# Kernel tuning notes

Hardware: AMD Instinct MI355X
Metric: run time of the kernel (lower is better)

Reference implementation:

```python
import jax, jax.numpy as jnp
import numpy as np

BLOCK = 64  # block_size from config
NEG_INF = -1e9


def setup_inputs() -> dict:
    key = jax.random.key(0)
    k1, k2, k3, k4 = jax.random.split(key, 4)
    B, H, S, D = 2, 8, 2048, 64
    nb = S // BLOCK  # 32 blocks per side
    query = jax.random.normal(k1, (B, H, S, D), dtype=jnp.float32)
    key_t = jax.random.normal(k2, (B, H, S, D), dtype=jnp.float32)
    value = jax.random.normal(k3, (B, H, S, D), dtype=jnp.float32)
    # binary block mask; force diagonal blocks on so every row has >=1 valid key
    mat = jax.random.randint(k4, (nb, nb), 0, 2).astype(jnp.int32)
    mat = mat.at[jnp.arange(nb), jnp.arange(nb)].set(1)
    mask = jnp.ones((B, S), dtype=jnp.float32)  # padding mask (1 = keep)
    return {"query": query, "key": key_t, "value": value, "mask": mask, "mat": mat}


def reference(query, key, value, mask, mat):
    # Upsample block mask [nb, nb] -> dense [S, S] (nearest, like nn.Upsample)
    block_dense = jnp.repeat(jnp.repeat(mat, BLOCK, axis=0), BLOCK, axis=1) > 0
    # Block-sparse QK^T: only positions inside nonzero blocks participate.
    scores = jnp.einsum('bhqd,bhkd->bhqk', query, key)
    # Additive padding-mask bias, as in the original: 1e6 * (1 - mask)
    scores = scores - 1e6 * (1.0 - mask)[:, None, None, :]
    # Positions outside the block pattern are excluded from the softmax.
    scores = jnp.where(block_dense[None, None, :, :], scores, NEG_INF)
    attn = jax.nn.softmax(scores, axis=-1)
    out = jnp.einsum('bhqk,bhkd->bhqd', attn, value)
    return out
```

## Files before the change

kernel.cpp:

```cpp
#include <hip/hip_runtime.h>


typedef __attribute__((ext_vector_type(8))) short short8;
typedef __attribute__((ext_vector_type(4))) short short4_;
typedef __attribute__((ext_vector_type(4))) float float4_;
typedef __attribute__((ext_vector_type(8))) _Float16 half8_;

#define B_   2
#define H_   8
#define S_   2048
#define D_   64
#define NB_  32
#define KP   72

__device__ __forceinline__ short f2bf(float f) {
    union { float f; unsigned int u; } x; x.f = f;
    unsigned int r = x.u + 0x7FFFu + ((x.u >> 16) & 1u);
    return (short)(r >> 16);
}
__device__ __forceinline__ float bf2f(short s) {
    union { unsigned int u; float f; } x; x.u = ((unsigned int)(unsigned short)s) << 16;
    return x.f;
}
__device__ __forceinline__ short f2h(float f) {
    _Float16 h = (_Float16)f;
    return __builtin_bit_cast(short, h);
}

__global__ __launch_bounds__(256)
void preconvert_kernel(const float* __restrict__ K, const float* __restrict__ V,
                       short* __restrict__ Khf, short* __restrict__ Vtb) {
    __shared__ short vn[64 * KP];
    const int tid = threadIdx.x;
    const int kt  = blockIdx.x;
    const int bh  = blockIdx.y;
    const size_t tb = ((size_t)bh * S_ + kt * 64) * D_;

#pragma unroll
    for (int it = 0; it < 4; ++it) {
        int i = tid + it * 256;
        int row = i >> 4, c4 = (i & 15) * 4;
        float4_ kv = *(const float4_*)(K + tb + row * D_ + c4);
        short4_ kh;
#pragma unroll
        for (int e = 0; e < 4; ++e) kh[e] = f2h(kv[e]);
        *(short4_*)(Khf + tb + row * D_ + c4) = kh;
        float4_ vv = *(const float4_*)(V + tb + row * D_ + c4);
        short4_ vb;
#pragma unroll
        for (int e = 0; e < 4; ++e) vb[e] = f2bf(vv[e]);
        *(short4_*)&vn[row * KP + c4] = vb;
    }
    __syncthreads();
#pragma unroll
    for (int it = 0; it < 2; ++it) {
        int i = tid + it * 256;
        int rowd = i >> 3, key8 = (i & 7) * 8;
        short8 o;
#pragma unroll
        for (int e = 0; e < 8; ++e) o[e] = vn[(key8 + e) * KP + rowd];
        *(short8*)(Vtb + (((size_t)(bh * NB_ + kt)) * 64 + rowd) * 64 + key8) = o;
    }
}

__global__ __launch_bounds__(128, 2)
void attn_mfma_h(const float* __restrict__ Q,
                 const float* __restrict__ Msk,
                 const int* __restrict__ Mat,
                 float* __restrict__ O,
                 const short* __restrict__ Khf_g,
                 const short* __restrict__ Vtb_g) {
    __shared__ __align__(16) short lds[(64 + 64 + 2 * 16) * KP];
    short* Kh = lds;
    short* Vt = lds + 64 * KP;
    short* Pl = lds + 2 * 64 * KP;

    const int tid  = threadIdx.x;
    const int wave = tid >> 6;
    const int lane = tid & 63;
    const int c    = lane & 15;
    const int quad = lane >> 4;

    const int qt = blockIdx.x;
    const int bh = blockIdx.y;
    const int b  = bh / H_;
    const int qb = qt >> 1;
    const size_t base = (size_t)bh * S_ * D_;

    half8_ qa0, qa1;
    {
        const float* qp = Q + base + (size_t)(qt * 32 + wave * 16 + c) * D_ + quad * 8;
#pragma unroll
        for (int e = 0; e < 8; ++e) {
            qa0[e] = (_Float16)qp[e];
            qa1[e] = (_Float16)qp[e + 32];
        }
    }

    float4_ o[4];
    float l_part[4];
#pragma unroll
    for (int t = 0; t < 4; ++t) { o[t][0] = 0.f; o[t][1] = 0.f; o[t][2] = 0.f; o[t][3] = 0.f; }
#pragma unroll
    for (int j = 0; j < 4; ++j) l_part[j] = 0.f;

    unsigned long long bm = __ballot(Mat[qb * NB_ + (lane & 31)] != 0);
    unsigned int mbits = (unsigned int)(bm & 0xFFFFFFFFull);

    int srow[4], scol[4];
#pragma unroll
    for (int it = 0; it < 4; ++it) {
        int i = tid + it * 128;
        srow[it] = i >> 3;
        scol[it] = (i & 7) * 8;
    }

    short8 sK[4], sV[4];
    float  biasn[4];

    int kb = __builtin_ctz(mbits);
    mbits &= mbits - 1;
    {
        const short* kh = Khf_g + base + (size_t)kb * 64 * D_;
        const short* vt = Vtb_g + ((size_t)(bh * NB_ + kb)) * 64 * 64;
#pragma unroll
        for (int it = 0; it < 4; ++it) {
            sK[it] = *(const short8*)(kh + srow[it] * 64 + scol[it]);
            sV[it] = *(const short8*)(vt + srow[it] * 64 + scol[it]);
        }
#pragma unroll
        for (int t = 0; t < 4; ++t)
            biasn[t] = -1.0e6f * (1.0f - Msk[(size_t)b * S_ + kb * 64 + t * 16 + c]);
    }

    for (;;) {
        __syncthreads();
#pragma unroll
        for (int it = 0; it < 4; ++it) {
            *(short8*)&Kh[srow[it] * KP + scol[it]] = sK[it];
            *(short8*)&Vt[srow[it] * KP + scol[it]] = sV[it];
        }
        float biasc[4];
#pragma unroll
        for (int t = 0; t < 4; ++t) biasc[t] = biasn[t];
        __syncthreads();

        const bool have_next = (mbits != 0);
        if (have_next) {
            kb = __builtin_ctz(mbits);
            mbits &= mbits - 1;
            const short* kh = Khf_g + base + (size_t)kb * 64 * D_;
            const short* vt = Vtb_g + ((size_t)(bh * NB_ + kb)) * 64 * 64;
#pragma unroll
            for (int it = 0; it < 4; ++it) {
                sK[it] = *(const short8*)(kh + srow[it] * 64 + scol[it]);
                sV[it] = *(const short8*)(vt + srow[it] * 64 + scol[it]);
            }
#pragma unroll
            for (int t = 0; t < 4; ++t)
                biasn[t] = -1.0e6f * (1.0f - Msk[(size_t)b * S_ + kb * 64 + t * 16 + c]);
        }

        float4_ sc[4];
#pragma unroll
        for (int t = 0; t < 4; ++t) { sc[t][0] = 0.f; sc[t][1] = 0.f; sc[t][2] = 0.f; sc[t][3] = 0.f; }
#pragma unroll
        for (int t = 0; t < 4; ++t) {
            const short* kp_ = &Kh[(t * 16 + c) * KP + quad * 8];
            half8_ kb0 = __builtin_bit_cast(half8_, *(const short8*)(kp_));
            half8_ kb1 = __builtin_bit_cast(half8_, *(const short8*)(kp_ + 32));
            sc[t] = __builtin_amdgcn_mfma_f32_16x16x32_f16(qa0, kb0, sc[t], 0, 0, 0);
            sc[t] = __builtin_amdgcn_mfma_f32_16x16x32_f16(qa1, kb1, sc[t], 0, 0, 0);
        }

        short* Pw = Pl + wave * 16 * KP;
#pragma unroll
        for (int t = 0; t < 4; ++t) {
#pragma unroll
            for (int j = 0; j < 4; ++j) {
                float p = __expf(sc[t][j] + biasc[t]);
                l_part[j] += p;
                Pw[(quad * 4 + j) * KP + t * 16 + c] = f2bf(p);
            }
        }

        const short* pp = Pl + wave * 16 * KP + c * KP + quad * 8;
        short8 pa0 = *(const short8*)(pp);
        short8 pa1 = *(const short8*)(pp + 32);

#pragma unroll
        for (int t = 0; t < 4; ++t) {
            const short* vp = &Vt[(t * 16 + c) * KP + quad * 8];
            short8 vb0 = *(const short8*)(vp);
            short8 vb1 = *(const short8*)(vp + 32);
            o[t] = __builtin_amdgcn_mfma_f32_16x16x32_bf16(pa0, vb0, o[t], 0, 0, 0);
            o[t] = __builtin_amdgcn_mfma_f32_16x16x32_bf16(pa1, vb1, o[t], 0, 0, 0);
        }

        if (!have_next) break;
    }

#pragma unroll
    for (int j = 0; j < 4; ++j) {
        float rs = l_part[j];
        rs += __shfl_xor(rs, 1);
        rs += __shfl_xor(rs, 2);
        rs += __shfl_xor(rs, 4);
        rs += __shfl_xor(rs, 8);
        float inv = 1.0f / rs;
        size_t rowoff = base + (size_t)(qt * 32 + wave * 16 + quad * 4 + j) * D_;
#pragma unroll
        for (int t = 0; t < 4; ++t)
            O[rowoff + t * 16 + c] = o[t][j] * inv;
    }
}

__global__ __launch_bounds__(256, 2)
void attn_mfma_fb(const float* __restrict__ Q,
                  const float* __restrict__ K,
                  const float* __restrict__ V,
                  const float* __restrict__ Msk,
                  const int* __restrict__ Mat,
                  float* __restrict__ O) {
    __shared__ __align__(16) short lds[4 * 64 * KP];
    short* Khi = lds;
    short* Klo = lds + 64 * KP;
    short* Vt  = lds + 2 * 64 * KP;
    short* Pl  = lds + 3 * 64 * KP;

    const int tid  = threadIdx.x;
    const int wave = tid >> 6;
    const int lane = tid & 63;
    const int c    = lane & 15;
    const int quad = lane >> 4;

    const int qb = blockIdx.x;
    const int bh = blockIdx.y;
    const int b  = bh / H_;
    const size_t base = (size_t)bh * S_ * D_;

    short8 qh0, qh1, ql0, ql1;
    {
        const float* qp = Q + base + (size_t)(qb * 64 + wave * 16 + c) * D_ + quad * 8;
#pragma unroll
        for (int e = 0; e < 8; ++e) {
            float f0 = qp[e], f1 = qp[e + 32];
            qh0[e] = f2bf(f0); ql0[e] = f2bf(f0 - bf2f(qh0[e]));
            qh1[e] = f2bf(f1); ql1[e] = f2bf(f1 - bf2f(qh1[e]));
        }
    }

    float4_ o[4];
    float l_part[4];
#pragma unroll
    for (int t = 0; t < 4; ++t) { o[t][0] = 0.f; o[t][1] = 0.f; o[t][2] = 0.f; o[t][3] = 0.f; }
#pragma unroll
    for (int j = 0; j < 4; ++j) l_part[j] = 0.f;

    for (int kb = 0; kb < NB_; ++kb) {
        if (Mat[qb * NB_ + kb] == 0) continue;

        __syncthreads();
        {
            const float* kg = K + base + (size_t)kb * 64 * D_;
            const float* vg = V + base + (size_t)kb * 64 * D_;
#pragma unroll
            for (int it = 0; it < 4; ++it) {
                int i = tid + it * 256;
                int row = i >> 4, c4 = (i & 15) * 4;
                float4_ kv = *(const float4_*)(kg + row * D_ + c4);
                short4_ hi, lo;
#pragma unroll
                for (int e = 0; e < 4; ++e) {
                    hi[e] = f2bf(kv[e]);
                    lo[e] = f2bf(kv[e] - bf2f(hi[e]));
                }
                *(short4_*)&Khi[row * KP + c4] = hi;
                *(short4_*)&Klo[row * KP + c4] = lo;
                float4_ vv = *(const float4_*)(vg + row * D_ + c4);
#pragma unroll
                for (int e = 0; e < 4; ++e) Vt[(c4 + e) * KP + row] = f2bf(vv[e]);
            }
        }
        __syncthreads();

        float4_ sc[4];
#pragma unroll
        for (int t = 0; t < 4; ++t) { sc[t][0] = 0.f; sc[t][1] = 0.f; sc[t][2] = 0.f; sc[t][3] = 0.f; }
#pragma unroll
        for (int t = 0; t < 4; ++t) {
            const short* kph = &Khi[(t * 16 + c) * KP + quad * 8];
            const short* kpl = &Klo[(t * 16 + c) * KP + quad * 8];
            short8 kh0 = *(const short8*)(kph);
            short8 kh1 = *(const short8*)(kph + 32);
            short8 kl0 = *(const short8*)(kpl);
            short8 kl1 = *(const short8*)(kpl + 32);
            sc[t] = __builtin_amdgcn_mfma_f32_16x16x32_bf16(qh0, kh0, sc[t], 0, 0, 0);
            sc[t] = __builtin_amdgcn_mfma_f32_16x16x32_bf16(qh1, kh1, sc[t], 0, 0, 0);
            sc[t] = __builtin_amdgcn_mfma_f32_16x16x32_bf16(qh0, kl0, sc[t], 0, 0, 0);
            sc[t] = __builtin_amdgcn_mfma_f32_16x16x32_bf16(qh1, kl1, sc[t], 0, 0, 0);
            sc[t] = __builtin_amdgcn_mfma_f32_16x16x32_bf16(ql0, kh0, sc[t], 0, 0, 0);
            sc[t] = __builtin_amdgcn_mfma_f32_16x16x32_bf16(ql1, kh1, sc[t], 0, 0, 0);
        }

        short* Pw = Pl + wave * 16 * KP;
#pragma unroll
        for (int t = 0; t < 4; ++t) {
            float bias = -1.0e6f * (1.0f - Msk[(size_t)b * S_ + kb * 64 + t * 16 + c]);
#pragma unroll
            for (int j = 0; j < 4; ++j) {
                float p = __expf(sc[t][j] + bias);
                l_part[j] += p;
                Pw[(quad * 4 + j) * KP + t * 16 + c] = f2bf(p);
            }
        }

        const short* pp = Pl + wave * 16 * KP + c * KP + quad * 8;
        short8 pa0 = *(const short8*)(pp);
        short8 pa1 = *(const short8*)(pp + 32);

#pragma unroll
        for (int t = 0; t < 4; ++t) {
            const short* vp = &Vt[(t * 16 + c) * KP + quad * 8];
            short8 vb0 = *(const short8*)(vp);
            short8 vb1 = *(const short8*)(vp + 32);
            o[t] = __builtin_amdgcn_mfma_f32_16x16x32_bf16(pa0, vb0, o[t], 0, 0, 0);
            o[t] = __builtin_amdgcn_mfma_f32_16x16x32_bf16(pa1, vb1, o[t], 0, 0, 0);
        }
    }

#pragma unroll
    for (int j = 0; j < 4; ++j) {
        float rs = l_part[j];
        rs += __shfl_xor(rs, 1);
        rs += __shfl_xor(rs, 2);
        rs += __shfl_xor(rs, 4);
        rs += __shfl_xor(rs, 8);
        float inv = 1.0f / rs;
        size_t rowoff = base + (size_t)(qb * 64 + wave * 16 + quad * 4 + j) * D_;
#pragma unroll
        for (int t = 0; t < 4; ++t)
            O[rowoff + t * 16 + c] = o[t][j] * inv;
    }
}

extern "C" void kernel_launch(void* const* d_in, const int* in_sizes, int n_in,
                              void* d_out, int out_size, void* d_ws, size_t ws_size,
                              hipStream_t stream) {
    const float* q   = (const float*)d_in[0];
    const float* k   = (const float*)d_in[1];
    const float* v   = (const float*)d_in[2];
    const float* msk = (const float*)d_in[3];
    const int*   mat = (const int*)d_in[4];
    float*       out = (float*)d_out;

    const size_t elems = (size_t)B_ * H_ * S_ * D_;
    const size_t need  = 2 * elems * sizeof(short);
    const int use_pre  = (ws_size >= need) ? 1 : 0;

    short* khf = (short*)d_ws;
    short* vtb = khf + elems;

    if (use_pre) {
        dim3 pgrid(NB_, B_ * H_);
        preconvert_kernel<<<pgrid, dim3(256), 0, stream>>>(k, v, khf, vtb);
        dim3 grid(S_ / 32, B_ * H_);
        attn_mfma_h<<<grid, dim3(128), 0, stream>>>(q, msk, mat, out, khf, vtb);
    } else {
        dim3 grid(NB_, B_ * H_);
        attn_mfma_fb<<<grid, dim3(256), 0, stream>>>(q, k, v, msk, mat, out);
    }
}
```

Baseline: 112.9 us.

## Double-buffer K/V tiles in LDS with XOR swizzle and exp2 softmax

Replaces the padded single-buffer LDS staging with two XOR-swizzled K/V buffers. The next tile is written into the alternate buffer after the current compute, so each iteration needs one barrier instead of two. The log2(e) factor is folded into the fp16 K conversion and the mask bias, which lets the kernel call exp2f in place of __expf. P is now converted to bf16 by truncation rather than round-to-nearest. LDS use grows, which may lower occupancy, and truncation slightly reduces accuracy.

```diff
diff --git a/kernel.cpp b/kernel.cpp
--- a/kernel.cpp
+++ b/kernel.cpp
@@ -12,12 +12,17 @@
 #define D_   64
 #define NB_  32
 #define KP   72
+#define LOG2E 1.4426950408889634f
 
 __device__ __forceinline__ short f2bf(float f) {
     union { float f; unsigned int u; } x; x.f = f;
     unsigned int r = x.u + 0x7FFFu + ((x.u >> 16) & 1u);
     return (short)(r >> 16);
 }
+__device__ __forceinline__ short f2bf_t(float f) {
+    union { float f; unsigned int u; } x; x.f = f;
+    return (short)(x.u >> 16);
+}
 __device__ __forceinline__ float bf2f(short s) {
     union { unsigned int u; float f; } x; x.u = ((unsigned int)(unsigned short)s) << 16;
     return x.f;
@@ -25,6 +30,9 @@
 __device__ __forceinline__ short f2h(float f) {
     _Float16 h = (_Float16)f;
     return __builtin_bit_cast(short, h);
+}
+__device__ __forceinline__ int swz(int row, int gran) {
+    return (row << 6) + (((gran ^ row) & 7) << 3);
 }
 
 __global__ __launch_bounds__(256)
@@ -43,7 +51,7 @@
         float4_ kv = *(const float4_*)(K + tb + row * D_ + c4);
         short4_ kh;
 #pragma unroll
-        for (int e = 0; e < 4; ++e) kh[e] = f2h(kv[e]);
+        for (int e = 0; e < 4; ++e) kh[e] = f2h(kv[e] * LOG2E);
         *(short4_*)(Khf + tb + row * D_ + c4) = kh;
         float4_ vv = *(const float4_*)(V + tb + row * D_ + c4);
         short4_ vb;
@@ -64,16 +72,13 @@
 }
 
 __global__ __launch_bounds__(128, 2)
-void attn_mfma_h(const float* __restrict__ Q,
-                 const float* __restrict__ Msk,
-                 const int* __restrict__ Mat,
-                 float* __restrict__ O,
-                 const short* __restrict__ Khf_g,
-                 const short* __restrict__ Vtb_g) {
-    __shared__ __align__(16) short lds[(64 + 64 + 2 * 16) * KP];
-    short* Kh = lds;
-    short* Vt = lds + 64 * KP;
-    short* Pl = lds + 2 * 64 * KP;
+void attn_mfma_db(const float* __restrict__ Q,
+                  const float* __restrict__ Msk,
+                  const int* __restrict__ Mat,
+                  float* __restrict__ O,
+                  const short* __restrict__ Khf_g,
+                  const short* __restrict__ Vtb_g) {
+    __shared__ __align__(16) short lds[4 * 4096 + 2 * 16 * KP];
 
     const int tid  = threadIdx.x;
     const int wave = tid >> 6;
@@ -104,15 +109,22 @@
 #pragma unroll
     for (int j = 0; j < 4; ++j) l_part[j] = 0.f;
 
-    unsigned long long bm = __ballot(Mat[qb * NB_ + (lane & 31)] != 0);
-    unsigned int mbits = (unsigned int)(bm & 0xFFFFFFFFull);
-
-    int srow[4], scol[4];
+    unsigned long long bmv = __ballot(Mat[qb * NB_ + (lane & 31)] != 0);
+    unsigned int mbits = (unsigned int)(bmv & 0xFFFFFFFFull);
+
+    int srow[4], sgrn[4], soff[4];
 #pragma unroll
     for (int it = 0; it < 4; ++it) {
         int i = tid + it * 128;
         srow[it] = i >> 3;
-        scol[it] = (i & 7) * 8;
+        sgrn[it] = i & 7;
+        soff[it] = swz(srow[it], sgrn[it]);
+    }
+    int foff_lo[4], foff_hi[4];
+#pragma unroll
+    for (int t = 0; t < 4; ++t) {
+        foff_lo[t] = swz(t * 16 + c, quad);
+        foff_hi[t] = swz(t * 16 + c, quad + 4);
     }
 
     short8 sK[4], sV[4];
@@ -125,25 +137,25 @@
         const short* vt = Vtb_g + ((size_t)(bh * NB_ + kb)) * 64 * 64;
 #pragma unroll
         for (int it = 0; it < 4; ++it) {
-            sK[it] = *(const short8*)(kh + srow[it] * 64 + scol[it]);
-            sV[it] = *(const short8*)(vt + srow[it] * 64 + scol[it]);
+            sK[it] = *(const short8*)(kh + srow[it] * 64 + sgrn[it] * 8);
+            sV[it] = *(const short8*)(vt + srow[it] * 64 + sgrn[it] * 8);
         }
 #pragma unroll
         for (int t = 0; t < 4; ++t)
-            biasn[t] = -1.0e6f * (1.0f - Msk[(size_t)b * S_ + kb * 64 + t * 16 + c]);
-    }
-
+            biasn[t] = -1.0e6f * LOG2E * (1.0f - Msk[(size_t)b * S_ + kb * 64 + t * 16 + c]);
+#pragma unroll
+        for (int it = 0; it < 4; ++it) {
+            *(short8*)&lds[soff[it]]        = sK[it];
+            *(short8*)&lds[8192 + soff[it]] = sV[it];
+        }
+    }
+    __syncthreads();
+
+    int pbo = 0;
     for (;;) {
-        __syncthreads();
-#pragma unroll
-        for (int it = 0; it < 4; ++it) {
-            *(short8*)&Kh[srow[it] * KP + scol[it]] = sK[it];
-            *(short8*)&Vt[srow[it] * KP + scol[it]] = sV[it];
-        }
         float biasc[4];
 #pragma unroll
         for (int t = 0; t < 4; ++t) biasc[t] = biasn[t];
-        __syncthreads();
 
         const bool have_next = (mbits != 0);
         if (have_next) {
@@ -153,12 +165,12 @@
             const short* vt = Vtb_g + ((size_t)(bh * NB_ + kb)) * 64 * 64;
 #pragma unroll
             for (int it = 0; it < 4; ++it) {
-                sK[it] = *(const short8*)(kh + srow[it] * 64 + scol[it]);
-                sV[it] = *(const short8*)(vt + srow[it] * 64 + scol[it]);
+                sK[it] = *(const short8*)(kh + srow[it] * 64 + sgrn[it] * 8);
+                sV[it] = *(const short8*)(vt + srow[it] * 64 + sgrn[it] * 8);
             }
 #pragma unroll
             for (int t = 0; t < 4; ++t)
-                biasn[t] = -1.0e6f * (1.0f - Msk[(size_t)b * S_ + kb * 64 + t * 16 + c]);
+                biasn[t] = -1.0e6f * LOG2E * (1.0f - Msk[(size_t)b * S_ + kb * 64 + t * 16 + c]);
         }
 
         float4_ sc[4];
@@ -166,38 +178,45 @@
         for (int t = 0; t < 4; ++t) { sc[t][0] = 0.f; sc[t][1] = 0.f; sc[t][2] = 0.f; sc[t][3] = 0.f; }
 #pragma unroll
         for (int t = 0; t < 4; ++t) {
-            const short* kp_ = &Kh[(t * 16 + c) * KP + quad * 8];
-            half8_ kb0 = __builtin_bit_cast(half8_, *(const short8*)(kp_));
-            half8_ kb1 = __builtin_bit_cast(half8_, *(const short8*)(kp_ + 32));
+            half8_ kb0 = __builtin_bit_cast(half8_, *(const short8*)&lds[pbo + foff_lo[t]]);
+            half8_ kb1 = __builtin_bit_cast(half8_, *(const short8*)&lds[pbo + foff_hi[t]]);
             sc[t] = __builtin_amdgcn_mfma_f32_16x16x32_f16(qa0, kb0, sc[t], 0, 0, 0);
             sc[t] = __builtin_amdgcn_mfma_f32_16x16x32_f16(qa1, kb1, sc[t], 0, 0, 0);
         }
 
-        short* Pw = Pl + wave * 16 * KP;
+        const int pwoff = 16384 + wave * 16 * KP;
 #pragma unroll
         for (int t = 0; t < 4; ++t) {
 #pragma unroll
             for (int j = 0; j < 4; ++j) {
-                float p = __expf(sc[t][j] + biasc[t]);
+                float p = exp2f(sc[t][j] + biasc[t]);
                 l_part[j] += p;
-                Pw[(quad * 4 + j) * KP + t * 16 + c] = f2bf(p);
+                lds[pwoff + (quad * 4 + j) * KP + t * 16 + c] = f2bf_t(p);
             }
         }
 
-        const short* pp = Pl + wave * 16 * KP + c * KP + quad * 8;
+        const short* pp = &lds[pwoff + c * KP + quad * 8];
         short8 pa0 = *(const short8*)(pp);
         short8 pa1 = *(const short8*)(pp + 32);
 
 #pragma unroll
         for (int t = 0; t < 4; ++t) {
-            const short* vp = &Vt[(t * 16 + c) * KP + quad * 8];
-            short8 vb0 = *(const short8*)(vp);
-            short8 vb1 = *(const short8*)(vp + 32);
+            short8 vb0 = *(const short8*)&lds[8192 + pbo + foff_lo[t]];
+            short8 vb1 = *(const short8*)&lds[8192 + pbo + foff_hi[t]];
             o[t] = __builtin_amdgcn_mfma_f32_16x16x32_bf16(pa0, vb0, o[t], 0, 0, 0);
             o[t] = __builtin_amdgcn_mfma_f32_16x16x32_bf16(pa1, vb1, o[t], 0, 0, 0);
         }
 
         if (!have_next) break;
+
+        const int nbo = pbo ^ 4096;
+#pragma unroll
+        for (int it = 0; it < 4; ++it) {
+            *(short8*)&lds[nbo + soff[it]]        = sK[it];
+            *(short8*)&lds[8192 + nbo + soff[it]] = sV[it];
+        }
+        __syncthreads();
+        pbo = nbo;
     }
 
 #pragma unroll
@@ -365,7 +384,7 @@
         dim3 pgrid(NB_, B_ * H_);
         preconvert_kernel<<<pgrid, dim3(256), 0, stream>>>(k, v, khf, vtb);
         dim3 grid(S_ / 32, B_ * H_);
-        attn_mfma_h<<<grid, dim3(128), 0, stream>>>(q, msk, mat, out, khf, vtb);
+        attn_mfma_db<<<grid, dim3(128), 0, stream>>>(q, msk, mat, out, khf, vtb);
     } else {
         dim3 grid(NB_, B_ * H_);
         attn_mfma_fb<<<grid, dim3(256), 0, stream>>>(q, k, v, msk, mat, out);
```

Result: no change. 113.2 us (+0.2%).
